# Kernel optimization log

Measured on AMD Instinct MI355X. Metric: run time of the kernel, lower is better.

## Reference

```python
import jax, jax.numpy as jnp
import numpy as np

# E2M1 (FP4) value table: low 3 bits magnitude, bit 3 sign (indices 8..15 negative)
FP4_TABLE = jnp.array([0.0, 0.5, 1.0, 1.5, 2.0, 3.0, 4.0, 6.0,
                       0.0, -0.5, -1.0, -1.5, -2.0, -3.0, -4.0, -6.0], dtype=jnp.float32)
FP4_BLOCK = 32  # per-row 1x32 scale groups


def dequant_fp4(packed, scale):
    """packed: [E, O, I//2] uint8 (two e2m1 nibbles per byte, low nibble first),
    scale: [E, O, I//32] float32 (e8m0, i.e. powers of two). Returns [E, O, I] float32."""
    lo = (packed & 15).astype(jnp.int32)
    hi = ((packed >> 4) & 15).astype(jnp.int32)
    # interleave low, high nibbles along the input dim (matches torch stack(...,-1).flatten)
    vals = FP4_TABLE[jnp.stack([lo, hi], axis=-1)]  # [E, O, I//2, 2]
    w = vals.reshape(packed.shape[0], packed.shape[1], packed.shape[2] * 2)
    return w * jnp.repeat(scale, FP4_BLOCK, axis=-1)


def setup_inputs() -> dict:
    T, H, F, E, K = 2048, 2048, 1024, 16, 4
    key = jax.random.key(0)
    k = jax.random.split(key, 8)
    hidden_states = jax.random.normal(k[0], (T, H), dtype=jnp.float32)
    topk_weights = jax.nn.softmax(jax.random.normal(k[1], (T, K)), axis=-1)
    topk_ids = jax.random.randint(k[2], (T, K), 0, E, dtype=jnp.int32)
    # checkpoint-native packed FP4 expert weights + e8m0 (power-of-two) scales
    gate_up_weight = jax.random.randint(k[3], (E, 2 * F, H // 2), 0, 256, dtype=jnp.int32).astype(jnp.uint8)
    gate_up_scale = jnp.exp2(jax.random.randint(k[4], (E, 2 * F, H // 32), -8, -5).astype(jnp.float32))
    down_weight = jax.random.randint(k[5], (E, H, F // 2), 0, 256, dtype=jnp.int32).astype(jnp.uint8)
    down_scale = jnp.exp2(jax.random.randint(k[6], (E, H, F // 32), -8, -5).astype(jnp.float32))
    return {"hidden_states": hidden_states, "topk_weights": topk_weights, "topk_ids": topk_ids,
            "gate_up_weight": gate_up_weight, "gate_up_scale": gate_up_scale,
            "down_weight": down_weight, "down_scale": down_scale}


def reference(hidden_states, topk_weights, topk_ids, gate_up_weight, gate_up_scale, down_weight, down_scale):
    # 1. dequantize checkpoint-native FP4 experts to dense float weights
    w_gate_up = dequant_fp4(gate_up_weight, gate_up_scale)  # [E, 2F, H]
    w_down = dequant_fp4(down_weight, down_scale)           # [E, H, F]
    T = hidden_states.shape[0]
    E = w_gate_up.shape[0]
    # 2. scatter routing weights into a dense [T, E] combine matrix
    combine = jnp.zeros((T, E), dtype=hidden_states.dtype)
    combine = combine.at[jnp.arange(T)[:, None], topk_ids].add(topk_weights)
    # 3. grouped expert GEMM (exact dense dispatch over experts)
    gu = jnp.einsum('th,eoh->teo', hidden_states, w_gate_up)  # [T, E, 2F]
    gate, up = jnp.split(gu, 2, axis=-1)                       # gate = first ffn_dim rows
    act = jax.nn.silu(gate) * up                               # SwiGLU (swiglu_limit=0 -> no clamping)
    act = act * combine[:, :, None]                            # fold routing weights into activations
    return jnp.einsum('tef,ehf->th', act, w_down)              # [T, H]
```

## Files before the change

kernel.cpp:

```cpp
#include <hip/hip_runtime.h>
#include <stdint.h>

#define HD 2048
#define FD 1024
#define NE 16
#define NPAIR 8192
#define BM 256
#define MAXT 48

typedef short bf16x8 __attribute__((ext_vector_type(8)));
typedef float f32x4 __attribute__((ext_vector_type(4)));
typedef unsigned short u16;

static __device__ __forceinline__ u16 f2bf(float f) {
  uint32_t u = __float_as_uint(f);
  u += 0x7FFFu + ((u >> 16) & 1u);
  return (u16)(u >> 16);
}

static __device__ __forceinline__ void sbar_cnt() {
  __builtin_amdgcn_sched_barrier(0);
  asm volatile("s_waitcnt vmcnt(5) lgkmcnt(0)" ::: "memory");
  __builtin_amdgcn_s_barrier();
  __builtin_amdgcn_sched_barrier(0);
}
static __device__ __forceinline__ void sbar_all() {
  __builtin_amdgcn_sched_barrier(0);
  asm volatile("s_waitcnt vmcnt(0) lgkmcnt(0)" ::: "memory");
  __builtin_amdgcn_s_barrier();
  __builtin_amdgcn_sched_barrier(0);
}

struct DqTab { uint32_t hA, hB, lA, lB; };

static __device__ __forceinline__ DqTab make_tab(uint32_t sbits) {
  int n = (int)(sbits >> 23) - 127;
  int q = n >> 1;
  uint32_t r = (uint32_t)(n & 1);
  uint32_t mq = (uint32_t)(-q);
  uint32_t sub1 = mq * 0x01010100u;
  uint32_t subA = mq * 0x01010101u;
  DqTab t;
  t.hA = (r ? 0x40403F00u : 0x3F3F3F00u) - sub1;
  t.hB = (r ? 0x41414040u : 0x40404040u) - subA;
  t.lA = r ? 0x40008000u : 0xC0800000u;
  t.lB = r ? 0x4000C080u : 0xC0804000u;
  return t;
}

static __device__ __forceinline__ void dq8(uint32_t p, const DqTab& t, uint32_t* d) {
  uint32_t a = p & 0x0F0F0F0Fu;
  uint32_t b = (p >> 4) & 0x0F0F0F0Fu;
  uint32_t x0 = __builtin_amdgcn_perm(b, a, 0x05010400u);
  uint32_t x1 = __builtin_amdgcn_perm(b, a, 0x07030602u);
  uint32_t m0 = x0 & 0x07070707u;
  uint32_t m1 = x1 & 0x07070707u;
  uint32_t h0 = __builtin_amdgcn_perm(t.hB, t.hA, m0) | ((x0 & 0x08080808u) << 4);
  uint32_t h1 = __builtin_amdgcn_perm(t.hB, t.hA, m1) | ((x1 & 0x08080808u) << 4);
  uint32_t l0 = __builtin_amdgcn_perm(t.lB, t.lA, m0);
  uint32_t l1 = __builtin_amdgcn_perm(t.lB, t.lA, m1);
  d[0] = __builtin_amdgcn_perm(h0, l0, 0x05010400u);
  d[1] = __builtin_amdgcn_perm(h0, l0, 0x07030602u);
  d[2] = __builtin_amdgcn_perm(h1, l1, 0x05010400u);
  d[3] = __builtin_amdgcn_perm(h1, l1, 0x07030602u);
}

static __device__ __forceinline__ uint32_t pack4(int4 v) {
  return (uint32_t)(v.x & 0xFF) | ((uint32_t)(v.y & 0xFF) << 8) |
         ((uint32_t)(v.z & 0xFF) << 16) | ((uint32_t)v.w << 24);
}

static __device__ __forceinline__ bf16x8 dqfrag(const uint32_t* pB, const uint32_t* pS,
                                                int row, int j, int q) {
  uint32_t pb = pB[row * 9 + j * 4 + q];
  DqTab t = make_tab(pS[row * 2 + j]);
  uint32_t d[4];
  dq8(pb, t, d);
  union { uint32_t u[4]; bf16x8 v; } cv;
  cv.u[0] = d[0]; cv.u[1] = d[1]; cv.u[2] = d[2]; cv.u[3] = d[3];
  return cv.v;
}

static __device__ __forceinline__ void glds16(const void* g, void* l) {
  __builtin_amdgcn_global_load_lds(
      (const __attribute__((address_space(1))) uint32_t*)g,
      (__attribute__((address_space(3))) uint32_t*)l, 16, 0, 0);
}

__global__ void cast_kernel(const float* __restrict__ x, u16* __restrict__ xb) {
  int i = blockIdx.x * 256 + threadIdx.x;
  float4 v = ((const float4*)x)[i];
  ushort4 o;
  o.x = f2bf(v.x); o.y = f2bf(v.y); o.z = f2bf(v.z); o.w = f2bf(v.w);
  ((ushort4*)xb)[i] = o;
}

__global__ void zero_kernel(float4* __restrict__ out) {
  out[blockIdx.x * 256 + threadIdx.x] = float4{0.f, 0.f, 0.f, 0.f};
}

__global__ void route_kernel(const int* __restrict__ ids, const float* __restrict__ tw,
                             int* __restrict__ rows, float* __restrict__ rw,
                             int* __restrict__ te, int* __restrict__ pidx) {
  __shared__ int cnt[NE], base[NE], run[NE];
  int tid = threadIdx.x;
  if (tid < NE) { cnt[tid] = 0; run[tid] = 0; }
  __syncthreads();
  for (int i = tid; i < NPAIR; i += 256) atomicAdd(&cnt[ids[i]], 1);
  __syncthreads();
  if (tid == 0) {
    int cum = 0;
    for (int e = 0; e < NE; ++e) {
      base[e] = cum;
      int nt = (cnt[e] + BM - 1) >> 8;
      for (int j = 0; j < nt; ++j) te[(cum >> 8) + j] = e;
      cum += nt << 8;
    }
    for (int t = cum >> 8; t < MAXT; ++t) te[t] = -1;
  }
  __syncthreads();
  for (int i = tid; i < MAXT * BM; i += 256) {
    rows[i] = -1;
    rw[i] = 0.f;
    if (pidx) pidx[i] = -1;
  }
  __syncthreads();
  for (int i = tid; i < NPAIR; i += 256) {
    int e = ids[i];
    int p = base[e] + atomicAdd(&run[e], 1);
    rows[p] = i >> 2;
    rw[p] = tw[i];
    if (pidx) pidx[p] = i;
  }
}

__global__ __launch_bounds__(256, 2) void gemm1_kernel(
    const u16* __restrict__ xb, const int* __restrict__ gup32,
    const uint32_t* __restrict__ gus, const int* __restrict__ rows,
    const float* __restrict__ rw, const int* __restrict__ te,
    u16* __restrict__ act) {
  const int tile = blockIdx.y;
  const int e = te[tile];
  if (e < 0) return;
  const int f0 = blockIdx.x * 64;

  __shared__ u16 sA[2][BM * 64];
  __shared__ uint32_t sBp[2][128 * 9];
  __shared__ uint32_t sSc[2][256];
  __shared__ int rows_s[BM];
  __shared__ float rw_s[BM];

  const int tid = threadIdx.x;
  rows_s[tid] = rows[tile * BM + tid];
  rw_s[tid] = rw[tile * BM + tid];
  __syncthreads();

  const int lane = tid & 63;
  const int w = tid >> 6;
  const int wr = w >> 1;
  const int wc = w & 1;
  const int q = lane >> 4, c = lane & 15;

  uint32_t aofs[8];
#pragma unroll
  for (int i = 0; i < 8; ++i) {
    const int lrow = w * 64 + i * 8 + (lane >> 3);
    int grow = rows_s[lrow];
    grow = grow < 0 ? 0 : grow;
    aofs[i] = (uint32_t)grow * HD + (uint32_t)(((lane & 7) ^ (lrow & 7)) << 3);
  }

  uint32_t obj[4];
#pragma unroll
  for (int j = 0; j < 4; ++j) {
    const int r_ = (tid >> 3) + j * 32;
    const int o_ = r_ < 64 ? f0 + r_ : 1024 + f0 + (r_ - 64);
    obj[j] = (uint32_t)(e * 2048 + o_) * 1024 + (uint32_t)((tid & 7) << 2);
  }
  const int r_sc = tid >> 1;
  const int o_sc = r_sc < 64 ? f0 + r_sc : 1024 + f0 + (r_sc - 64);
  const uint32_t scb = (uint32_t)(e * 2048 + o_sc) * 64 + (uint32_t)(tid & 1);

  const int x0 = ((q * 16) ^ ((c & 7) << 4)) >> 1;
  const int x1 = ((64 + q * 16) ^ ((c & 7) << 4)) >> 1;

  f32x4 Cg[8][2], Cu[8][2];
#pragma unroll
  for (int s = 0; s < 8; ++s)
#pragma unroll
    for (int t2 = 0; t2 < 2; ++t2) {
      Cg[s][t2] = f32x4{0.f, 0.f, 0.f, 0.f};
      Cu[s][t2] = f32x4{0.f, 0.f, 0.f, 0.f};
    }

  int4 breg[4];
  uint32_t sreg;

  {
#pragma unroll
    for (int i = 0; i < 8; ++i)
      glds16(xb + aofs[i], &sA[0][(w * 64 + i * 8) * 64]);
    int4 b0[4];
#pragma unroll
    for (int j = 0; j < 4; ++j) b0[j] = *(const int4*)(gup32 + obj[j]);
    uint32_t s0 = gus[scb];
#pragma unroll
    for (int j = 0; j < 4; ++j)
      sBp[0][((tid >> 3) + j * 32) * 9 + (tid & 7)] = pack4(b0[j]);
    sSc[0][tid] = s0;
#pragma unroll
    for (int j = 0; j < 4; ++j) breg[j] = *(const int4*)(gup32 + obj[j] + 32);
    sreg = gus[scb + 2];
    sbar_all();
  }

  for (int s = 0; s < 32; ++s) {
    const int cur = s & 1;
    if (s < 31) {
#pragma unroll
      for (int i = 0; i < 8; ++i)
        glds16(xb + aofs[i] + (uint32_t)(s + 1) * 64, &sA[cur ^ 1][(w * 64 + i * 8) * 64]);
#pragma unroll
      for (int j = 0; j < 4; ++j)
        sBp[cur ^ 1][((tid >> 3) + j * 32) * 9 + (tid & 7)] = pack4(breg[j]);
      sSc[cur ^ 1][tid] = sreg;
    }
    __builtin_amdgcn_sched_barrier(0);
    if (s < 30) {
#pragma unroll
      for (int j = 0; j < 4; ++j)
        breg[j] = *(const int4*)(gup32 + obj[j] + (uint32_t)(s + 2) * 32);
      sreg = gus[scb + (uint32_t)(s + 2) * 2];
    }
#pragma unroll
    for (int j = 0; j < 2; ++j) {
      const int xo = j ? x1 : x0;
      bf16x8 bg[2], bu[2];
#pragma unroll
      for (int t2 = 0; t2 < 2; ++t2) {
        bg[t2] = dqfrag(sBp[cur], sSc[cur], wc * 32 + t2 * 16 + c, j, q);
        bu[t2] = dqfrag(sBp[cur], sSc[cur], 64 + wc * 32 + t2 * 16 + c, j, q);
      }
#pragma unroll
      for (int s4 = 0; s4 < 8; ++s4) {
        bf16x8 af = *(const bf16x8*)&sA[cur][(wr * 128 + s4 * 16 + c) * 64 + xo];
#pragma unroll
        for (int t2 = 0; t2 < 2; ++t2) {
          Cg[s4][t2] = __builtin_amdgcn_mfma_f32_16x16x32_bf16(af, bg[t2], Cg[s4][t2], 0, 0, 0);
          Cu[s4][t2] = __builtin_amdgcn_mfma_f32_16x16x32_bf16(af, bu[t2], Cu[s4][t2], 0, 0, 0);
        }
      }
    }
    if (s < 30) sbar_cnt(); else sbar_all();
  }

#pragma unroll
  for (int s4 = 0; s4 < 8; ++s4) {
    const int mlb = wr * 128 + s4 * 16 + q * 4;
#pragma unroll
    for (int t2 = 0; t2 < 2; ++t2) {
      const int fg = f0 + wc * 32 + t2 * 16 + c;
#pragma unroll
      for (int r = 0; r < 4; ++r) {
        const int ml = mlb + r;
        float g = Cg[s4][t2][r];
        float u = Cu[s4][t2][r];
        float aval = g / (1.f + __expf(-g)) * u * rw_s[ml];
        act[(size_t)(tile * BM + ml) * FD + fg] = f2bf(aval);
      }
    }
  }
}

__global__ __launch_bounds__(256, 2) void gemm2_kernel(
    const u16* __restrict__ act, const int* __restrict__ dwn32,
    const uint32_t* __restrict__ dsc, const int* __restrict__ rows,
    const int* __restrict__ pidx, const int* __restrict__ te,
    float* __restrict__ out, float* __restrict__ pout) {
  const int tile = blockIdx.y;
  const int e = te[tile];
  if (e < 0) return;
  const int h0 = blockIdx.x * 128;

  __shared__ u16 sA[2][BM * 64];
  __shared__ uint32_t sBp[2][128 * 9];
  __shared__ uint32_t sSc[2][256];
  __shared__ int rows_s[BM];
  __shared__ int pidx_s[BM];

  const int tid = threadIdx.x;
  rows_s[tid] = rows[tile * BM + tid];
  pidx_s[tid] = pout ? pidx[tile * BM + tid] : -1;
  __syncthreads();

  const int lane = tid & 63;
  const int w = tid >> 6;
  const int wr = w >> 1;
  const int wc = w & 1;
  const int q = lane >> 4, c = lane & 15;

  uint32_t aofs[8];
#pragma unroll
  for (int i = 0; i < 8; ++i) {
    const int lrow = w * 64 + i * 8 + (lane >> 3);
    aofs[i] = (uint32_t)(tile * BM + lrow) * FD + (uint32_t)(((lane & 7) ^ (lrow & 7)) << 3);
  }

  uint32_t obj[4];
#pragma unroll
  for (int j = 0; j < 4; ++j) {
    const int r_ = (tid >> 3) + j * 32;
    obj[j] = (uint32_t)(e * 2048 + h0 + r_) * 512 + (uint32_t)((tid & 7) << 2);
  }
  const uint32_t scb = (uint32_t)(e * 2048 + h0 + (tid >> 1)) * 32 + (uint32_t)(tid & 1);

  const int x0 = ((q * 16) ^ ((c & 7) << 4)) >> 1;
  const int x1 = ((64 + q * 16) ^ ((c & 7) << 4)) >> 1;

  f32x4 Cd[8][4];
#pragma unroll
  for (int s = 0; s < 8; ++s)
#pragma unroll
    for (int t2 = 0; t2 < 4; ++t2) Cd[s][t2] = f32x4{0.f, 0.f, 0.f, 0.f};

  int4 breg[4];
  uint32_t sreg;

  {
#pragma unroll
    for (int i = 0; i < 8; ++i)
      glds16(act + aofs[i], &sA[0][(w * 64 + i * 8) * 64]);
    int4 b0[4];
#pragma unroll
    for (int j = 0; j < 4; ++j) b0[j] = *(const int4*)(dwn32 + obj[j]);
    uint32_t s0 = dsc[scb];
#pragma unroll
    for (int j = 0; j < 4; ++j)
      sBp[0][((tid >> 3) + j * 32) * 9 + (tid & 7)] = pack4(b0[j]);
    sSc[0][tid] = s0;
#pragma unroll
    for (int j = 0; j < 4; ++j) breg[j] = *(const int4*)(dwn32 + obj[j] + 32);
    sreg = dsc[scb + 2];
    sbar_all();
  }

  for (int s = 0; s < 16; ++s) {
    const int cur = s & 1;
    if (s < 15) {
#pragma unroll
      for (int i = 0; i < 8; ++i)
        glds16(act + aofs[i] + (uint32_t)(s + 1) * 64, &sA[cur ^ 1][(w * 64 + i * 8) * 64]);
#pragma unroll
      for (int j = 0; j < 4; ++j)
        sBp[cur ^ 1][((tid >> 3) + j * 32) * 9 + (tid & 7)] = pack4(breg[j]);
      sSc[cur ^ 1][tid] = sreg;
    }
    __builtin_amdgcn_sched_barrier(0);
    if (s < 14) {
#pragma unroll
      for (int j = 0; j < 4; ++j)
        breg[j] = *(const int4*)(dwn32 + obj[j] + (uint32_t)(s + 2) * 32);
      sreg = dsc[scb + (uint32_t)(s + 2) * 2];
    }
#pragma unroll
    for (int j = 0; j < 2; ++j) {
      const int xo = j ? x1 : x0;
      bf16x8 bf_[4];
#pragma unroll
      for (int t2 = 0; t2 < 4; ++t2)
        bf_[t2] = dqfrag(sBp[cur], sSc[cur], wc * 64 + t2 * 16 + c, j, q);
#pragma unroll
      for (int s4 = 0; s4 < 8; ++s4) {
        bf16x8 af = *(const bf16x8*)&sA[cur][(wr * 128 + s4 * 16 + c) * 64 + xo];
#pragma unroll
        for (int t2 = 0; t2 < 4; ++t2)
          Cd[s4][t2] = __builtin_amdgcn_mfma_f32_16x16x32_bf16(af, bf_[t2], Cd[s4][t2], 0, 0, 0);
      }
    }
    if (s < 14) sbar_cnt(); else sbar_all();
  }

  if (pout) {
#pragma unroll
    for (int s4 = 0; s4 < 8; ++s4) {
      const int mlb = wr * 128 + s4 * 16 + q * 4;
#pragma unroll
      for (int t2 = 0; t2 < 4; ++t2) {
        const int hg = h0 + wc * 64 + t2 * 16 + c;
#pragma unroll
        for (int r = 0; r < 4; ++r) {
          int prow = pidx_s[mlb + r];
          if (prow >= 0) pout[(size_t)prow * HD + hg] = Cd[s4][t2][r];
        }
      }
    }
  } else {
#pragma unroll
    for (int s4 = 0; s4 < 8; ++s4) {
      const int mlb = wr * 128 + s4 * 16 + q * 4;
#pragma unroll
      for (int t2 = 0; t2 < 4; ++t2) {
        const int hg = h0 + wc * 64 + t2 * 16 + c;
#pragma unroll
        for (int r = 0; r < 4; ++r) {
          int token = rows_s[mlb + r];
          if (token >= 0) atomicAdd(&out[(size_t)token * HD + hg], Cd[s4][t2][r]);
        }
      }
    }
  }
}

__global__ void finalize_kernel(const float4* __restrict__ pout, float4* __restrict__ out) {
  int j = blockIdx.x * 256 + threadIdx.x;
  int token = j >> 9;
  int col = j & 511;
  const float4* p = pout + ((size_t)token * 4) * 512 + col;
  float4 a = p[0], b = p[512], c = p[1024], d = p[1536];
  out[j] = float4{a.x + b.x + c.x + d.x, a.y + b.y + c.y + d.y,
                  a.z + b.z + c.z + d.z, a.w + b.w + c.w + d.w};
}

extern "C" void kernel_launch(void* const* d_in, const int* in_sizes, int n_in,
                              void* d_out, int out_size, void* d_ws, size_t ws_size,
                              hipStream_t stream) {
  const float* hidden = (const float*)d_in[0];
  const float* tw = (const float*)d_in[1];
  const int* ids = (const int*)d_in[2];
  const int* gup32 = (const int*)d_in[3];
  const uint32_t* gus = (const uint32_t*)d_in[4];
  const int* dwn32 = (const int*)d_in[5];
  const uint32_t* dsc = (const uint32_t*)d_in[6];
  float* out = (float*)d_out;

  char* ws = (char*)d_ws;
  int* rows = (int*)(ws);
  float* rw = (float*)(ws + 49152);
  int* te = (int*)(ws + 98304);
  u16* xb = (u16*)(ws + 131072);
  u16* act = (u16*)(ws + 8519680);

  const size_t POUT_OFF = 33685504ULL;
  const size_t PIDX_OFF = POUT_OFF + (size_t)NPAIR * HD * 4;
  const size_t WS_NEED = PIDX_OFF + (size_t)MAXT * BM * 4;
  const bool big = ws_size >= WS_NEED;
  float* pout = big ? (float*)(ws + POUT_OFF) : nullptr;
  int* pidx = big ? (int*)(ws + PIDX_OFF) : nullptr;

  cast_kernel<<<dim3(4096), dim3(256), 0, stream>>>(hidden, xb);
  if (!big) zero_kernel<<<dim3(4096), dim3(256), 0, stream>>>((float4*)out);
  route_kernel<<<dim3(1), dim3(256), 0, stream>>>(ids, tw, rows, rw, te, pidx);
  gemm1_kernel<<<dim3(16, MAXT), dim3(256), 0, stream>>>(xb, gup32, gus, rows, rw, te, act);
  gemm2_kernel<<<dim3(16, MAXT), dim3(256), 0, stream>>>(act, dwn32, dsc, rows, pidx, te, out, pout);
  if (big) finalize_kernel<<<dim3(1024 * 1024 / 256), dim3(256), 0, stream>>>((const float4*)pout, (float4*)out);
}
```

Before: 488.3 us.

## Pre-pack FP4 weights into dense words and use atomic output accumulation

Adds a repack kernel that compresses the byte-per-int32 FP4 weight inputs into packed 32-bit words in workspace, once per call. Both grouped GEMMs then fetch one 16-byte vector per thread per stage instead of four, with a matching lighter vmcnt wait. This cuts the weight bytes each expert tile reads and removes the pack work from the inner loop, at the cost of a full extra pass over both weight tensors every call. The per-pair partial-output buffer and finalize reduction are also dropped in favour of zeroing the output and accumulating with float atomics, which adds atomic contention and makes the summation order nondeterministic.

```diff
diff --git a/kernel.cpp b/kernel.cpp
--- a/kernel.cpp
+++ b/kernel.cpp
@@ -18,9 +18,15 @@
   return (u16)(u >> 16);
 }
 
-static __device__ __forceinline__ void sbar_cnt() {
+static __device__ __forceinline__ void sbar_cnt5() {
   __builtin_amdgcn_sched_barrier(0);
   asm volatile("s_waitcnt vmcnt(5) lgkmcnt(0)" ::: "memory");
+  __builtin_amdgcn_s_barrier();
+  __builtin_amdgcn_sched_barrier(0);
+}
+static __device__ __forceinline__ void sbar_cnt2() {
+  __builtin_amdgcn_sched_barrier(0);
+  asm volatile("s_waitcnt vmcnt(2) lgkmcnt(0)" ::: "memory");
   __builtin_amdgcn_s_barrier();
   __builtin_amdgcn_sched_barrier(0);
 }
@@ -99,9 +105,22 @@
   out[blockIdx.x * 256 + threadIdx.x] = float4{0.f, 0.f, 0.f, 0.f};
 }
 
+__global__ void repack_kernel(const int* __restrict__ g, const int* __restrict__ d,
+                              uint32_t* __restrict__ gp, uint32_t* __restrict__ dp) {
+  int i = blockIdx.x * 256 + threadIdx.x;
+  if (i < 8388608) {
+    int4 v = ((const int4*)g)[i];
+    gp[i] = pack4(v);
+  } else {
+    int j = i - 8388608;
+    int4 v = ((const int4*)d)[j];
+    dp[j] = pack4(v);
+  }
+}
+
 __global__ void route_kernel(const int* __restrict__ ids, const float* __restrict__ tw,
                              int* __restrict__ rows, float* __restrict__ rw,
-                             int* __restrict__ te, int* __restrict__ pidx) {
+                             int* __restrict__ te) {
   __shared__ int cnt[NE], base[NE], run[NE];
   int tid = threadIdx.x;
   if (tid < NE) { cnt[tid] = 0; run[tid] = 0; }
@@ -119,26 +138,22 @@
     for (int t = cum >> 8; t < MAXT; ++t) te[t] = -1;
   }
   __syncthreads();
-  for (int i = tid; i < MAXT * BM; i += 256) {
-    rows[i] = -1;
-    rw[i] = 0.f;
-    if (pidx) pidx[i] = -1;
-  }
+  for (int i = tid; i < MAXT * BM; i += 256) { rows[i] = -1; rw[i] = 0.f; }
   __syncthreads();
   for (int i = tid; i < NPAIR; i += 256) {
     int e = ids[i];
     int p = base[e] + atomicAdd(&run[e], 1);
     rows[p] = i >> 2;
     rw[p] = tw[i];
-    if (pidx) pidx[p] = i;
-  }
-}
-
-__global__ __launch_bounds__(256, 2) void gemm1_kernel(
+  }
+}
+
+template <bool PK>
+__global__ __launch_bounds__(256, 2) void gemm1_t(
     const u16* __restrict__ xb, const int* __restrict__ gup32,
-    const uint32_t* __restrict__ gus, const int* __restrict__ rows,
-    const float* __restrict__ rw, const int* __restrict__ te,
-    u16* __restrict__ act) {
+    const uint32_t* __restrict__ gpk, const uint32_t* __restrict__ gus,
+    const int* __restrict__ rows, const float* __restrict__ rw,
+    const int* __restrict__ te, u16* __restrict__ act) {
   const int tile = blockIdx.y;
   const int e = te[tile];
   if (e < 0) return;
@@ -171,11 +186,19 @@
   }
 
   uint32_t obj[4];
-#pragma unroll
-  for (int j = 0; j < 4; ++j) {
-    const int r_ = (tid >> 3) + j * 32;
-    const int o_ = r_ < 64 ? f0 + r_ : 1024 + f0 + (r_ - 64);
-    obj[j] = (uint32_t)(e * 2048 + o_) * 1024 + (uint32_t)((tid & 7) << 2);
+  uint32_t pkb = 0;
+  int pr = 0, ph = 0;
+  if constexpr (PK) {
+    pr = tid >> 1; ph = tid & 1;
+    const int o_ = pr < 64 ? f0 + pr : 1024 + f0 + (pr - 64);
+    pkb = (uint32_t)(e * 2048 + o_) * 256 + (uint32_t)(ph * 4);
+  } else {
+#pragma unroll
+    for (int j = 0; j < 4; ++j) {
+      const int r_ = (tid >> 3) + j * 32;
+      const int o_ = r_ < 64 ? f0 + r_ : 1024 + f0 + (r_ - 64);
+      obj[j] = (uint32_t)(e * 2048 + o_) * 1024 + (uint32_t)((tid & 7) << 2);
+    }
   }
   const int r_sc = tid >> 1;
   const int o_sc = r_sc < 64 ? f0 + r_sc : 1024 + f0 + (r_sc - 64);
@@ -194,23 +217,35 @@
     }
 
   int4 breg[4];
+  uint4 bpk;
   uint32_t sreg;
 
   {
 #pragma unroll
     for (int i = 0; i < 8; ++i)
       glds16(xb + aofs[i], &sA[0][(w * 64 + i * 8) * 64]);
-    int4 b0[4];
-#pragma unroll
-    for (int j = 0; j < 4; ++j) b0[j] = *(const int4*)(gup32 + obj[j]);
-    uint32_t s0 = gus[scb];
-#pragma unroll
-    for (int j = 0; j < 4; ++j)
-      sBp[0][((tid >> 3) + j * 32) * 9 + (tid & 7)] = pack4(b0[j]);
-    sSc[0][tid] = s0;
-#pragma unroll
-    for (int j = 0; j < 4; ++j) breg[j] = *(const int4*)(gup32 + obj[j] + 32);
-    sreg = gus[scb + 2];
+    if constexpr (PK) {
+      uint4 b0 = *(const uint4*)(gpk + pkb);
+      sBp[0][pr * 9 + ph * 4 + 0] = b0.x;
+      sBp[0][pr * 9 + ph * 4 + 1] = b0.y;
+      sBp[0][pr * 9 + ph * 4 + 2] = b0.z;
+      sBp[0][pr * 9 + ph * 4 + 3] = b0.w;
+      sSc[0][tid] = gus[scb];
+      bpk = *(const uint4*)(gpk + pkb + 8);
+      sreg = gus[scb + 2];
+    } else {
+      int4 b0[4];
+#pragma unroll
+      for (int j = 0; j < 4; ++j) b0[j] = *(const int4*)(gup32 + obj[j]);
+      uint32_t s0 = gus[scb];
+#pragma unroll
+      for (int j = 0; j < 4; ++j)
+        sBp[0][((tid >> 3) + j * 32) * 9 + (tid & 7)] = pack4(b0[j]);
+      sSc[0][tid] = s0;
+#pragma unroll
+      for (int j = 0; j < 4; ++j) breg[j] = *(const int4*)(gup32 + obj[j] + 32);
+      sreg = gus[scb + 2];
+    }
     sbar_all();
   }
 
@@ -220,16 +255,27 @@
 #pragma unroll
       for (int i = 0; i < 8; ++i)
         glds16(xb + aofs[i] + (uint32_t)(s + 1) * 64, &sA[cur ^ 1][(w * 64 + i * 8) * 64]);
-#pragma unroll
-      for (int j = 0; j < 4; ++j)
-        sBp[cur ^ 1][((tid >> 3) + j * 32) * 9 + (tid & 7)] = pack4(breg[j]);
+      if constexpr (PK) {
+        sBp[cur ^ 1][pr * 9 + ph * 4 + 0] = bpk.x;
+        sBp[cur ^ 1][pr * 9 + ph * 4 + 1] = bpk.y;
+        sBp[cur ^ 1][pr * 9 + ph * 4 + 2] = bpk.z;
+        sBp[cur ^ 1][pr * 9 + ph * 4 + 3] = bpk.w;
+      } else {
+#pragma unroll
+        for (int j = 0; j < 4; ++j)
+          sBp[cur ^ 1][((tid >> 3) + j * 32) * 9 + (tid & 7)] = pack4(breg[j]);
+      }
       sSc[cur ^ 1][tid] = sreg;
     }
     __builtin_amdgcn_sched_barrier(0);
     if (s < 30) {
-#pragma unroll
-      for (int j = 0; j < 4; ++j)
-        breg[j] = *(const int4*)(gup32 + obj[j] + (uint32_t)(s + 2) * 32);
+      if constexpr (PK) {
+        bpk = *(const uint4*)(gpk + pkb + (uint32_t)(s + 2) * 8);
+      } else {
+#pragma unroll
+        for (int j = 0; j < 4; ++j)
+          breg[j] = *(const int4*)(gup32 + obj[j] + (uint32_t)(s + 2) * 32);
+      }
       sreg = gus[scb + (uint32_t)(s + 2) * 2];
     }
 #pragma unroll
@@ -251,7 +297,8 @@
         }
       }
     }
-    if (s < 30) sbar_cnt(); else sbar_all();
+    if (s < 30) { if constexpr (PK) sbar_cnt2(); else sbar_cnt5(); }
+    else sbar_all();
   }
 
 #pragma unroll
@@ -272,11 +319,12 @@
   }
 }
 
-__global__ __launch_bounds__(256, 2) void gemm2_kernel(
+template <bool PK>
+__global__ __launch_bounds__(256, 2) void gemm2_t(
     const u16* __restrict__ act, const int* __restrict__ dwn32,
-    const uint32_t* __restrict__ dsc, const int* __restrict__ rows,
-    const int* __restrict__ pidx, const int* __restrict__ te,
-    float* __restrict__ out, float* __restrict__ pout) {
+    const uint32_t* __restrict__ dpk, const uint32_t* __restrict__ dsc,
+    const int* __restrict__ rows, const int* __restrict__ te,
+    float* __restrict__ out) {
   const int tile = blockIdx.y;
   const int e = te[tile];
   if (e < 0) return;
@@ -286,11 +334,9 @@
   __shared__ uint32_t sBp[2][128 * 9];
   __shared__ uint32_t sSc[2][256];
   __shared__ int rows_s[BM];
-  __shared__ int pidx_s[BM];
 
   const int tid = threadIdx.x;
   rows_s[tid] = rows[tile * BM + tid];
-  pidx_s[tid] = pout ? pidx[tile * BM + tid] : -1;
   __syncthreads();
 
   const int lane = tid & 63;
@@ -307,10 +353,17 @@
   }
 
   uint32_t obj[4];
-#pragma unroll
-  for (int j = 0; j < 4; ++j) {
-    const int r_ = (tid >> 3) + j * 32;
-    obj[j] = (uint32_t)(e * 2048 + h0 + r_) * 512 + (uint32_t)((tid & 7) << 2);
+  uint32_t pkb = 0;
+  int pr = 0, ph = 0;
+  if constexpr (PK) {
+    pr = tid >> 1; ph = tid & 1;
+    pkb = (uint32_t)(e * 2048 + h0 + pr) * 128 + (uint32_t)(ph * 4);
+  } else {
+#pragma unroll
+    for (int j = 0; j < 4; ++j) {
+      const int r_ = (tid >> 3) + j * 32;
+      obj[j] = (uint32_t)(e * 2048 + h0 + r_) * 512 + (uint32_t)((tid & 7) << 2);
+    }
   }
   const uint32_t scb = (uint32_t)(e * 2048 + h0 + (tid >> 1)) * 32 + (uint32_t)(tid & 1);
 
@@ -324,23 +377,35 @@
     for (int t2 = 0; t2 < 4; ++t2) Cd[s][t2] = f32x4{0.f, 0.f, 0.f, 0.f};
 
   int4 breg[4];
+  uint4 bpk;
   uint32_t sreg;
 
   {
 #pragma unroll
     for (int i = 0; i < 8; ++i)
       glds16(act + aofs[i], &sA[0][(w * 64 + i * 8) * 64]);
-    int4 b0[4];
-#pragma unroll
-    for (int j = 0; j < 4; ++j) b0[j] = *(const int4*)(dwn32 + obj[j]);
-    uint32_t s0 = dsc[scb];
-#pragma unroll
-    for (int j = 0; j < 4; ++j)
-      sBp[0][((tid >> 3) + j * 32) * 9 + (tid & 7)] = pack4(b0[j]);
-    sSc[0][tid] = s0;
-#pragma unroll
-    for (int j = 0; j < 4; ++j) breg[j] = *(const int4*)(dwn32 + obj[j] + 32);
-    sreg = dsc[scb + 2];
+    if constexpr (PK) {
+      uint4 b0 = *(const uint4*)(dpk + pkb);
+      sBp[0][pr * 9 + ph * 4 + 0] = b0.x;
+      sBp[0][pr * 9 + ph * 4 + 1] = b0.y;
+      sBp[0][pr * 9 + ph * 4 + 2] = b0.z;
+      sBp[0][pr * 9 + ph * 4 + 3] = b0.w;
+      sSc[0][tid] = dsc[scb];
+      bpk = *(const uint4*)(dpk + pkb + 8);
+      sreg = dsc[scb + 2];
+    } else {
+      int4 b0[4];
+#pragma unroll
+      for (int j = 0; j < 4; ++j) b0[j] = *(const int4*)(dwn32 + obj[j]);
+      uint32_t s0 = dsc[scb];
+#pragma unroll
+      for (int j = 0; j < 4; ++j)
+        sBp[0][((tid >> 3) + j * 32) * 9 + (tid & 7)] = pack4(b0[j]);
+      sSc[0][tid] = s0;
+#pragma unroll
+      for (int j = 0; j < 4; ++j) breg[j] = *(const int4*)(dwn32 + obj[j] + 32);
+      sreg = dsc[scb + 2];
+    }
     sbar_all();
   }
 
@@ -350,16 +415,27 @@
 #pragma unroll
       for (int i = 0; i < 8; ++i)
         glds16(act + aofs[i] + (uint32_t)(s + 1) * 64, &sA[cur ^ 1][(w * 64 + i * 8) * 64]);
-#pragma unroll
-      for (int j = 0; j < 4; ++j)
-        sBp[cur ^ 1][((tid >> 3) + j * 32) * 9 + (tid & 7)] = pack4(breg[j]);
+      if constexpr (PK) {
+        sBp[cur ^ 1][pr * 9 + ph * 4 + 0] = bpk.x;
+        sBp[cur ^ 1][pr * 9 + ph * 4 + 1] = bpk.y;
+        sBp[cur ^ 1][pr * 9 + ph * 4 + 2] = bpk.z;
+        sBp[cur ^ 1][pr * 9 + ph * 4 + 3] = bpk.w;
+      } else {
+#pragma unroll
+        for (int j = 0; j < 4; ++j)
+          sBp[cur ^ 1][((tid >> 3) + j * 32) * 9 + (tid & 7)] = pack4(breg[j]);
+      }
       sSc[cur ^ 1][tid] = sreg;
     }
     __builtin_amdgcn_sched_barrier(0);
     if (s < 14) {
-#pragma unroll
-      for (int j = 0; j < 4; ++j)
-        breg[j] = *(const int4*)(dwn32 + obj[j] + (uint32_t)(s + 2) * 32);
+      if constexpr (PK) {
+        bpk = *(const uint4*)(dpk + pkb + (uint32_t)(s + 2) * 8);
+      } else {
+#pragma unroll
+        for (int j = 0; j < 4; ++j)
+          breg[j] = *(const int4*)(dwn32 + obj[j] + (uint32_t)(s + 2) * 32);
+      }
       sreg = dsc[scb + (uint32_t)(s + 2) * 2];
     }
 #pragma unroll
@@ -377,48 +453,23 @@
           Cd[s4][t2] = __builtin_amdgcn_mfma_f32_16x16x32_bf16(af, bf_[t2], Cd[s4][t2], 0, 0, 0);
       }
     }
-    if (s < 14) sbar_cnt(); else sbar_all();
-  }
-
-  if (pout) {
-#pragma unroll
-    for (int s4 = 0; s4 < 8; ++s4) {
-      const int mlb = wr * 128 + s4 * 16 + q * 4;
-#pragma unroll
-      for (int t2 = 0; t2 < 4; ++t2) {
-        const int hg = h0 + wc * 64 + t2 * 16 + c;
-#pragma unroll
-        for (int r = 0; r < 4; ++r) {
-          int prow = pidx_s[mlb + r];
-          if (prow >= 0) pout[(size_t)prow * HD + hg] = Cd[s4][t2][r];
-        }
-      }
-    }
-  } else {
-#pragma unroll
-    for (int s4 = 0; s4 < 8; ++s4) {
-      const int mlb = wr * 128 + s4 * 16 + q * 4;
-#pragma unroll
-      for (int t2 = 0; t2 < 4; ++t2) {
-        const int hg = h0 + wc * 64 + t2 * 16 + c;
-#pragma unroll
-        for (int r = 0; r < 4; ++r) {
-          int token = rows_s[mlb + r];
-          if (token >= 0) atomicAdd(&out[(size_t)token * HD + hg], Cd[s4][t2][r]);
-        }
-      }
-    }
-  }
-}
-
-__global__ void finalize_kernel(const float4* __restrict__ pout, float4* __restrict__ out) {
-  int j = blockIdx.x * 256 + threadIdx.x;
-  int token = j >> 9;
-  int col = j & 511;
-  const float4* p = pout + ((size_t)token * 4) * 512 + col;
-  float4 a = p[0], b = p[512], c = p[1024], d = p[1536];
-  out[j] = float4{a.x + b.x + c.x + d.x, a.y + b.y + c.y + d.y,
-                  a.z + b.z + c.z + d.z, a.w + b.w + c.w + d.w};
+    if (s < 14) { if constexpr (PK) sbar_cnt2(); else sbar_cnt5(); }
+    else sbar_all();
+  }
+
+#pragma unroll
+  for (int s4 = 0; s4 < 8; ++s4) {
+    const int mlb = wr * 128 + s4 * 16 + q * 4;
+#pragma unroll
+    for (int t2 = 0; t2 < 4; ++t2) {
+      const int hg = h0 + wc * 64 + t2 * 16 + c;
+#pragma unroll
+      for (int r = 0; r < 4; ++r) {
+        int token = rows_s[mlb + r];
+        if (token >= 0) atomicAdd(&out[(size_t)token * HD + hg], Cd[s4][t2][r]);
+      }
+    }
+  }
 }
 
 extern "C" void kernel_launch(void* const* d_in, const int* in_sizes, int n_in,
@@ -440,17 +491,22 @@
   u16* xb = (u16*)(ws + 131072);
   u16* act = (u16*)(ws + 8519680);
 
-  const size_t POUT_OFF = 33685504ULL;
-  const size_t PIDX_OFF = POUT_OFF + (size_t)NPAIR * HD * 4;
-  const size_t WS_NEED = PIDX_OFF + (size_t)MAXT * BM * 4;
-  const bool big = ws_size >= WS_NEED;
-  float* pout = big ? (float*)(ws + POUT_OFF) : nullptr;
-  int* pidx = big ? (int*)(ws + PIDX_OFF) : nullptr;
+  const size_t GPK_OFF = 33685504ULL;
+  const size_t DPK_OFF = GPK_OFF + 33554432ULL;
+  const size_t WS_PK = DPK_OFF + 16777216ULL;
+  const bool pk = ws_size >= WS_PK;
+  uint32_t* gpk = (uint32_t*)(ws + GPK_OFF);
+  uint32_t* dpk = (uint32_t*)(ws + DPK_OFF);
 
   cast_kernel<<<dim3(4096), dim3(256), 0, stream>>>(hidden, xb);
-  if (!big) zero_kernel<<<dim3(4096), dim3(256), 0, stream>>>((float4*)out);
-  route_kernel<<<dim3(1), dim3(256), 0, stream>>>(ids, tw, rows, rw, te, pidx);
-  gemm1_kernel<<<dim3(16, MAXT), dim3(256), 0, stream>>>(xb, gup32, gus, rows, rw, te, act);
-  gemm2_kernel<<<dim3(16, MAXT), dim3(256), 0, stream>>>(act, dwn32, dsc, rows, pidx, te, out, pout);
-  if (big) finalize_kernel<<<dim3(1024 * 1024 / 256), dim3(256), 0, stream>>>((const float4*)pout, (float4*)out);
-}
+  zero_kernel<<<dim3(4096), dim3(256), 0, stream>>>((float4*)out);
+  route_kernel<<<dim3(1), dim3(256), 0, stream>>>(ids, tw, rows, rw, te);
+  if (pk) {
+    repack_kernel<<<dim3(49152), dim3(256), 0, stream>>>(gup32, dwn32, gpk, dpk);
+    gemm1_t<true><<<dim3(16, MAXT), dim3(256), 0, stream>>>(xb, gup32, gpk, gus, rows, rw, te, act);
+    gemm2_t<true><<<dim3(16, MAXT), dim3(256), 0, stream>>>(act, dwn32, dpk, dsc, rows, te, out);
+  } else {
+    gemm1_t<false><<<dim3(16, MAXT), dim3(256), 0, stream>>>(xb, gup32, gpk, gus, rows, rw, te, act);
+    gemm2_t<false><<<dim3(16, MAXT), dim3(256), 0, stream>>>(act, dwn32, dpk, dsc, rows, te, out);
+  }
+}
```

After: 554.3 us. 13.5% more time.
